# Kernel tuning notes

Measured on AMD Instinct MI355X. Metric: run time of the kernel, lower is better.

## Reference

```python
import jax, jax.numpy as jnp
import numpy as np

B, F, H1, H2, C = 8192, 256, 64, 32, 10  # batch, features, hidden1, hidden2, classes


def setup_inputs() -> dict:
    key = jax.random.key(0)
    ks = jax.random.split(key, 7)
    x = jax.random.normal(ks[0], (B, F), dtype=jnp.float32)
    # Per-feature stacked MLP params (xavier-ish scale)
    W1 = jax.random.normal(ks[1], (F, 1, H1), dtype=jnp.float32) * (2.0 / (1 + H1)) ** 0.5
    b1 = jnp.zeros((F, H1), dtype=jnp.float32)
    W2 = jax.random.normal(ks[2], (F, H1, H2), dtype=jnp.float32) * (2.0 / (H1 + H2)) ** 0.5
    b2 = jnp.zeros((F, H2), dtype=jnp.float32)
    Wout = jax.random.normal(ks[3], (F, H2, C), dtype=jnp.float32) * (2.0 / (H2 + C)) ** 0.5
    bias = jnp.zeros((C,), dtype=jnp.float32)
    return {"x": x, "W1": W1, "b1": b1, "W2": W2, "b2": b2, "Wout": Wout, "bias": bias}


def reference(x, W1, b1, W2, b2, Wout, bias):
    # Each feature f gets its own MLP: 1 -> H1 (ReLU) -> H2 (ReLU) -> C (no bias).
    # First layer input is x[:, f] unsqueezed to [B, 1]; since in-dim is 1 it is
    # an outer product: h1[b,f,:] = relu(x[b,f] * W1[f,0,:] + b1[f,:]).
    h1 = jax.nn.relu(x[:, :, None] * W1[:, 0, :][None, :, :] + b1[None, :, :])  # [B,F,H1]
    h2 = jax.nn.relu(jnp.einsum('bfh,fho->bfo', h1, W2) + b2[None, :, :])        # [B,F,H2]
    per_feat = jnp.einsum('bfo,foc->bfc', h2, Wout)                              # [B,F,C]
    # NAM: sum feature contributions + global bias (dropouts are 0 -> identity)
    return per_feat.sum(axis=1) + bias  # [B,C]
```

## Files before the change

### kernel.cpp

```cpp
#include <hip/hip_runtime.h>


#define NB 8192
#define NF 256
#define H1 64
#define H2 32
#define NC 10
#define THREADS 256
#define TS 64

__global__ __launch_bounds__(256) void nam_transpose(const float* __restrict__ x,
                                                     float* __restrict__ xT) {
    __shared__ float tile[TS][TS + 1];
    const int t  = threadIdx.x;
    const int c0 = t & 63;
    const int r0 = t >> 6;
    const int bb = blockIdx.x * TS;
    const int fb = blockIdx.y * TS;
#pragma unroll
    for (int k = 0; k < 16; ++k) {
        const int r = r0 + k * 4;
        tile[r][c0] = x[(size_t)(bb + r) * NF + fb + c0];
    }
    __syncthreads();
#pragma unroll
    for (int k = 0; k < 16; ++k) {
        const int r = r0 + k * 4;
        xT[(size_t)(fb + r) * NB + bb + c0] = tile[c0][r];
    }
}

template <int FPG>
__global__ __launch_bounds__(THREADS) void nam_core_v2(
    const float* __restrict__ xT, const float* __restrict__ W1,
    const float* __restrict__ b1, const float* __restrict__ W2,
    const float* __restrict__ b2, const float* __restrict__ Wout,
    float* __restrict__ partial) {
    const int fg = blockIdx.x;
    const int rg = blockIdx.y;
    const int b  = rg * THREADS + threadIdx.x;
    const int f0 = fg * FPG;

    float acc[NC];
#pragma unroll
    for (int c = 0; c < NC; ++c) acc[c] = 0.f;

#pragma unroll 1
    for (int ff = 0; ff < FPG; ++ff) {
        const int f = f0 + ff;
        const float xv = xT[(size_t)f * NB + b];
        const float* __restrict__ W1f = W1 + (size_t)f * H1;
        const float* __restrict__ b1f = b1 + (size_t)f * H1;
        const float* __restrict__ W2f = W2 + (size_t)f * (H1 * H2);
        const float* __restrict__ b2f = b2 + (size_t)f * H2;
        const float* __restrict__ Wof = Wout + (size_t)f * (H2 * NC);

        float h2[H2];
#pragma unroll
        for (int o = 0; o < H2; ++o) h2[o] = b2f[o];

#pragma unroll 8
        for (int hh = 0; hh < H1; ++hh) {
            const float a = fmaxf(fmaf(xv, W1f[hh], b1f[hh]), 0.f);
            const float* wr = W2f + (size_t)hh * H2;
#pragma unroll
            for (int o = 0; o < H2; ++o)
                h2[o] = fmaf(a, wr[o], h2[o]);
        }

#pragma unroll 8
        for (int o = 0; o < H2; ++o) {
            const float g = fmaxf(h2[o], 0.f);
            const float* wo = Wof + o * NC;
#pragma unroll
            for (int c = 0; c < NC; ++c)
                acc[c] = fmaf(g, wo[c], acc[c]);
        }
    }

#pragma unroll
    for (int c = 0; c < NC; ++c)
        partial[((size_t)fg * NC + c) * NB + b] = acc[c];
}

template <int G>
__global__ __launch_bounds__(256) void nam_reduce4(const float* __restrict__ part,
                                                   const float* __restrict__ bias,
                                                   float* __restrict__ out) {
    const int i  = blockIdx.x * 256 + threadIdx.x;
    const int c  = i / (NB / 4);
    const int b4 = i % (NB / 4);
    const float bc = bias[c];
    float4 s = {bc, bc, bc, bc};
#pragma unroll 8
    for (int g = 0; g < G; ++g) {
        const float4 v = ((const float4*)(part + ((size_t)g * NC + c) * NB))[b4];
        s.x += v.x; s.y += v.y; s.z += v.z; s.w += v.w;
    }
    const int b = 4 * b4;
    out[(size_t)(b + 0) * NC + c] = s.x;
    out[(size_t)(b + 1) * NC + c] = s.y;
    out[(size_t)(b + 2) * NC + c] = s.z;
    out[(size_t)(b + 3) * NC + c] = s.w;
}

__global__ __launch_bounds__(256) void nam_init_out(const float* __restrict__ bias,
                                                    float* __restrict__ out) {
    const int i = blockIdx.x * 256 + threadIdx.x;
    if (i < NB * NC) out[i] = bias[i % NC];
}

__global__ __launch_bounds__(256) void nam_fallback(
    const float* __restrict__ x,  const float* __restrict__ W1,
    const float* __restrict__ b1, const float* __restrict__ W2,
    const float* __restrict__ b2, const float* __restrict__ Wout,
    float* __restrict__ out) {
    const int b  = blockIdx.x * 256 + threadIdx.x;
    const int f0 = blockIdx.y * 16;
    float acc[NC];
#pragma unroll
    for (int c = 0; c < NC; ++c) acc[c] = 0.f;
#pragma unroll 1
    for (int ff = 0; ff < 16; ++ff) {
        const int f = f0 + ff;
        const float xv = x[(size_t)b * NF + f];
        const float* W1f = W1 + (size_t)f * H1;
        const float* b1f = b1 + (size_t)f * H1;
        const float* W2f = W2 + (size_t)f * (H1 * H2);
        const float* b2f = b2 + (size_t)f * H2;
        const float* Wof = Wout + (size_t)f * (H2 * NC);
        float h2[H2];
#pragma unroll
        for (int o = 0; o < H2; ++o) h2[o] = b2f[o];
#pragma unroll 8
        for (int hh = 0; hh < H1; ++hh) {
            const float a = fmaxf(fmaf(xv, W1f[hh], b1f[hh]), 0.f);
            const float* wr = W2f + (size_t)hh * H2;
#pragma unroll
            for (int o = 0; o < H2; ++o) h2[o] = fmaf(a, wr[o], h2[o]);
        }
#pragma unroll
        for (int o = 0; o < H2; ++o) {
            const float g = fmaxf(h2[o], 0.f);
            const float* wo = Wof + o * NC;
#pragma unroll
            for (int c = 0; c < NC; ++c) acc[c] = fmaf(g, wo[c], acc[c]);
        }
    }
    float* orow = out + (size_t)b * NC;
#pragma unroll
    for (int c = 0; c < NC; ++c) atomicAdd(&orow[c], acc[c]);
}

extern "C" void kernel_launch(void* const* d_in, const int* in_sizes, int n_in,
                              void* d_out, int out_size, void* d_ws, size_t ws_size,
                              hipStream_t stream) {
    const float* x    = (const float*)d_in[0];
    const float* W1   = (const float*)d_in[1];
    const float* b1   = (const float*)d_in[2];
    const float* W2   = (const float*)d_in[3];
    const float* b2   = (const float*)d_in[4];
    const float* Wout = (const float*)d_in[5];
    const float* bias = (const float*)d_in[6];
    float* out = (float*)d_out;

    float* xT   = (float*)d_ws;
    float* part = xT + (size_t)NF * NB;
    const size_t need2 = ((size_t)NF * NB + (size_t)128 * NC * NB) * sizeof(float);
    const size_t need4 = ((size_t)NF * NB + (size_t)64  * NC * NB) * sizeof(float);
    const int nred = (NC * NB / 4 + 255) / 256;

    if (ws_size >= need2) {
        nam_transpose<<<dim3(NB / TS, NF / TS), 256, 0, stream>>>(x, xT);
        nam_core_v2<2><<<dim3(128, NB / THREADS), THREADS, 0, stream>>>(
            xT, W1, b1, W2, b2, Wout, part);
        nam_reduce4<128><<<nred, 256, 0, stream>>>(part, bias, out);
    } else if (ws_size >= need4) {
        nam_transpose<<<dim3(NB / TS, NF / TS), 256, 0, stream>>>(x, xT);
        nam_core_v2<4><<<dim3(64, NB / THREADS), THREADS, 0, stream>>>(
            xT, W1, b1, W2, b2, Wout, part);
        nam_reduce4<64><<<nred, 256, 0, stream>>>(part, bias, out);
    } else {
        nam_init_out<<<(NB * NC + 255) / 256, 256, 0, stream>>>(bias, out);
        nam_fallback<<<dim3(NB / 256, 16), 256, 0, stream>>>(x, W1, b1, W2, b2, Wout, out);
    }
}
```

Measured before the change: 179.8 us.

## Split hidden-2 accumulation into halves, use 4 features per block, two-stage reduce

The core kernel now computes the 32 hidden-2 outputs in two chunks of 16, which lowers register pressure and may raise occupancy. The price is that the first-layer activations are recomputed for each chunk. The core kernel is also fixed at 4 features per block, halving the partial-sum buffer. The final reduction is split into two kernels, a parallel partial reduce over 8 chunks and then a final sum with bias, to expose more parallelism than the serial 64- or 128-way loop. This adds one kernel launch and an intermediate buffer.

New measurement: 211.7 us. 17.7% more time.

```diff
diff --git a/kernel.cpp b/kernel.cpp
--- a/kernel.cpp
+++ b/kernel.cpp
@@ -8,6 +8,9 @@
 #define NC 10
 #define THREADS 256
 #define TS 64
+#define FPG 4
+#define NFG (NF / FPG)
+#define GC 8
 
 __global__ __launch_bounds__(256) void nam_transpose(const float* __restrict__ x,
                                                      float* __restrict__ xT) {
@@ -30,8 +33,7 @@
     }
 }
 
-template <int FPG>
-__global__ __launch_bounds__(THREADS) void nam_core_v2(
+__global__ __launch_bounds__(THREADS) void nam_core_v3(
     const float* __restrict__ xT, const float* __restrict__ W1,
     const float* __restrict__ b1, const float* __restrict__ W2,
     const float* __restrict__ b2, const float* __restrict__ Wout,
@@ -55,26 +57,30 @@
         const float* __restrict__ b2f = b2 + (size_t)f * H2;
         const float* __restrict__ Wof = Wout + (size_t)f * (H2 * NC);
 
-        float h2[H2];
-#pragma unroll
-        for (int o = 0; o < H2; ++o) h2[o] = b2f[o];
+#pragma unroll
+        for (int ch = 0; ch < 2; ++ch) {
+            const int ob = ch * 16;
+            float h2[16];
+#pragma unroll
+            for (int o = 0; o < 16; ++o) h2[o] = b2f[ob + o];
 
 #pragma unroll 8
-        for (int hh = 0; hh < H1; ++hh) {
-            const float a = fmaxf(fmaf(xv, W1f[hh], b1f[hh]), 0.f);
-            const float* wr = W2f + (size_t)hh * H2;
-#pragma unroll
-            for (int o = 0; o < H2; ++o)
-                h2[o] = fmaf(a, wr[o], h2[o]);
-        }
+            for (int hh = 0; hh < H1; ++hh) {
+                const float a = fmaxf(fmaf(xv, W1f[hh], b1f[hh]), 0.f);
+                const float* wr = W2f + (size_t)hh * H2 + ob;
+#pragma unroll
+                for (int o = 0; o < 16; ++o)
+                    h2[o] = fmaf(a, wr[o], h2[o]);
+            }
 
 #pragma unroll 8
-        for (int o = 0; o < H2; ++o) {
-            const float g = fmaxf(h2[o], 0.f);
-            const float* wo = Wof + o * NC;
-#pragma unroll
-            for (int c = 0; c < NC; ++c)
-                acc[c] = fmaf(g, wo[c], acc[c]);
+            for (int o = 0; o < 16; ++o) {
+                const float g = fmaxf(h2[o], 0.f);
+                const float* wo = Wof + (size_t)(ob + o) * NC;
+#pragma unroll
+                for (int c = 0; c < NC; ++c)
+                    acc[c] = fmaf(g, wo[c], acc[c]);
+            }
         }
     }
 
@@ -83,8 +89,24 @@
         partial[((size_t)fg * NC + c) * NB + b] = acc[c];
 }
 
-template <int G>
-__global__ __launch_bounds__(256) void nam_reduce4(const float* __restrict__ part,
+__global__ __launch_bounds__(256) void nam_reduceA(const float* __restrict__ part,
+                                                   float* __restrict__ mid) {
+    const int i = blockIdx.x * 256 + threadIdx.x;
+    const int chunk = i / (NC * NB / 4);
+    const int j     = i % (NC * NB / 4);
+    const int c  = j / (NB / 4);
+    const int b4 = j % (NB / 4);
+    float4 s = {0.f, 0.f, 0.f, 0.f};
+#pragma unroll
+    for (int g = 0; g < NFG / GC; ++g) {
+        const float4 v =
+            ((const float4*)(part + ((size_t)(chunk * (NFG / GC) + g) * NC + c) * NB))[b4];
+        s.x += v.x; s.y += v.y; s.z += v.z; s.w += v.w;
+    }
+    ((float4*)(mid + ((size_t)chunk * NC + c) * NB))[b4] = s;
+}
+
+__global__ __launch_bounds__(256) void nam_reduceB(const float* __restrict__ mid,
                                                    const float* __restrict__ bias,
                                                    float* __restrict__ out) {
     const int i  = blockIdx.x * 256 + threadIdx.x;
@@ -92,9 +114,9 @@
     const int b4 = i % (NB / 4);
     const float bc = bias[c];
     float4 s = {bc, bc, bc, bc};
-#pragma unroll 8
-    for (int g = 0; g < G; ++g) {
-        const float4 v = ((const float4*)(part + ((size_t)g * NC + c) * NB))[b4];
+#pragma unroll
+    for (int g = 0; g < GC; ++g) {
+        const float4 v = ((const float4*)(mid + ((size_t)g * NC + c) * NB))[b4];
         s.x += v.x; s.y += v.y; s.z += v.z; s.w += v.w;
     }
     const int b = 4 * b4;
@@ -129,22 +151,26 @@
         const float* W2f = W2 + (size_t)f * (H1 * H2);
         const float* b2f = b2 + (size_t)f * H2;
         const float* Wof = Wout + (size_t)f * (H2 * NC);
-        float h2[H2];
-#pragma unroll
-        for (int o = 0; o < H2; ++o) h2[o] = b2f[o];
+#pragma unroll
+        for (int ch = 0; ch < 2; ++ch) {
+            const int ob = ch * 16;
+            float h2[16];
+#pragma unroll
+            for (int o = 0; o < 16; ++o) h2[o] = b2f[ob + o];
 #pragma unroll 8
-        for (int hh = 0; hh < H1; ++hh) {
-            const float a = fmaxf(fmaf(xv, W1f[hh], b1f[hh]), 0.f);
-            const float* wr = W2f + (size_t)hh * H2;
-#pragma unroll
-            for (int o = 0; o < H2; ++o) h2[o] = fmaf(a, wr[o], h2[o]);
-        }
-#pragma unroll
-        for (int o = 0; o < H2; ++o) {
-            const float g = fmaxf(h2[o], 0.f);
-            const float* wo = Wof + o * NC;
-#pragma unroll
-            for (int c = 0; c < NC; ++c) acc[c] = fmaf(g, wo[c], acc[c]);
+            for (int hh = 0; hh < H1; ++hh) {
+                const float a = fmaxf(fmaf(xv, W1f[hh], b1f[hh]), 0.f);
+                const float* wr = W2f + (size_t)hh * H2 + ob;
+#pragma unroll
+                for (int o = 0; o < 16; ++o) h2[o] = fmaf(a, wr[o], h2[o]);
+            }
+#pragma unroll
+            for (int o = 0; o < 16; ++o) {
+                const float g = fmaxf(h2[o], 0.f);
+                const float* wo = Wof + (size_t)(ob + o) * NC;
+#pragma unroll
+                for (int c = 0; c < NC; ++c) acc[c] = fmaf(g, wo[c], acc[c]);
+            }
         }
     }
     float* orow = out + (size_t)b * NC;
@@ -166,20 +192,16 @@
 
     float* xT   = (float*)d_ws;
     float* part = xT + (size_t)NF * NB;
-    const size_t need2 = ((size_t)NF * NB + (size_t)128 * NC * NB) * sizeof(float);
-    const size_t need4 = ((size_t)NF * NB + (size_t)64  * NC * NB) * sizeof(float);
-    const int nred = (NC * NB / 4 + 255) / 256;
-
-    if (ws_size >= need2) {
+    float* mid  = part + (size_t)NFG * NC * NB;
+    const size_t need =
+        ((size_t)NF * NB + (size_t)NFG * NC * NB + (size_t)GC * NC * NB) * sizeof(float);
+
+    if (ws_size >= need) {
         nam_transpose<<<dim3(NB / TS, NF / TS), 256, 0, stream>>>(x, xT);
-        nam_core_v2<2><<<dim3(128, NB / THREADS), THREADS, 0, stream>>>(
+        nam_core_v3<<<dim3(NFG, NB / THREADS), THREADS, 0, stream>>>(
             xT, W1, b1, W2, b2, Wout, part);
-        nam_reduce4<128><<<nred, 256, 0, stream>>>(part, bias, out);
-    } else if (ws_size >= need4) {
-        nam_transpose<<<dim3(NB / TS, NF / TS), 256, 0, stream>>>(x, xT);
-        nam_core_v2<4><<<dim3(64, NB / THREADS), THREADS, 0, stream>>>(
-            xT, W1, b1, W2, b2, Wout, part);
-        nam_reduce4<64><<<nred, 256, 0, stream>>>(part, bias, out);
+        nam_reduceA<<<GC * (NC * NB / 4) / 256, 256, 0, stream>>>(part, mid);
+        nam_reduceB<<<(NC * NB / 4) / 256, 256, 0, stream>>>(mid, bias, out);
     } else {
         nam_init_out<<<(NB * NC + 255) / 256, 256, 0, stream>>>(bias, out);
         nam_fallback<<<dim3(NB / 256, 16), 256, 0, stream>>>(x, W1, b1, W2, b2, Wout, out);
```
